# Kernel tuning notes

Measured on AMD Instinct MI355X. Metric: run time of the kernel, lower is better.

## Reference

```python
import jax, jax.numpy as jnp
import numpy as np

T = 100      # sequence length / output times
B = 2048     # batch
DT = 0.02    # euler step == spacing of ts -> one step per interval
CLAMP = 6.0
LOG2PI = float(np.log(2.0 * np.pi))
sp = jax.nn.softplus


def setup_inputs() -> dict:
    key = jax.random.key(0)
    ks = jax.random.split(key, 20)
    rn = lambda k, s, sc=1.0: jax.random.normal(k, s, dtype=jnp.float32) * sc
    inp = {}
    inp['xs'] = rn(ks[0], (T, B, 3, 50))
    inp['ts'] = jnp.arange(T, dtype=jnp.float32) * DT
    inp['eps0'] = rn(ks[1], (B, 6))
    inp['dW'] = rn(ks[2], (T - 1, B, 6)) * np.sqrt(DT)  # Brownian increments ~ N(0, dt)
    # encoder: 150->30->30->15
    inp['eW1'] = rn(ks[3], (150, 30), 150 ** -0.5); inp['eb1'] = jnp.zeros((30,), jnp.float32)
    inp['eW2'] = rn(ks[4], (30, 30), 30 ** -0.5);   inp['eb2'] = jnp.zeros((30,), jnp.float32)
    inp['eW3'] = rn(ks[5], (30, 15), 30 ** -0.5);   inp['eb3'] = jnp.zeros((15,), jnp.float32)
    # decoder: 6->30->30->100
    inp['dcW1'] = rn(ks[6], (6, 30), 6 ** -0.5);    inp['dcb1'] = jnp.zeros((30,), jnp.float32)
    inp['dcW2'] = rn(ks[7], (30, 30), 30 ** -0.5);  inp['dcb2'] = jnp.zeros((30,), jnp.float32)
    inp['dcW3'] = rn(ks[8], (30, 100), 30 ** -0.5); inp['dcb3'] = jnp.zeros((100,), jnp.float32)
    # f_net: (6+1+3)=10 -> 30 -> 6
    inp['fW1'] = rn(ks[9], (10, 30), 10 ** -0.5);   inp['fb1'] = jnp.zeros((30,), jnp.float32)
    inp['fW2'] = rn(ks[10], (30, 6), 30 ** -0.5);   inp['fb2'] = jnp.zeros((6,), jnp.float32)
    # h_net: (6+1)=7 -> 30 -> 6
    inp['hW1'] = rn(ks[11], (7, 30), 7 ** -0.5);    inp['hb1'] = jnp.zeros((30,), jnp.float32)
    inp['hW2'] = rn(ks[12], (30, 6), 30 ** -0.5);   inp['hb2'] = jnp.zeros((6,), jnp.float32)
    # 6 g_nets stacked: 2 -> 30 -> 1 (sigmoid)
    inp['gW1'] = rn(ks[13], (6, 2, 30), 2 ** -0.5); inp['gb1'] = jnp.zeros((6, 30), jnp.float32)
    inp['gW2'] = rn(ks[14], (6, 30, 1), 30 ** -0.5); inp['gb2'] = jnp.zeros((6, 1), jnp.float32)
    inp['pz0_mean'] = jnp.zeros((1, 6), jnp.float32)
    inp['pz0_logstd'] = jnp.zeros((1, 6), jnp.float32)
    return inp


def _forward(xs, ts, eps0, dW, eW1, eb1, eW2, eb2, eW3, eb3,
             dcW1, dcb1, dcW2, dcb2, dcW3, dcb3,
             fW1, fb1, fW2, fb2, hW1, hb1, hW2, hb2,
             gW1, gb1, gW2, gb2, pz0_mean, pz0_logstd):
    # ---- encoder on time-reversed xs ----
    xse = jnp.flip(xs, 0).reshape(T, B, 150)
    e = sp(xse @ eW1 + eb1)
    e = sp(e @ eW2 + eb2)
    e = e @ eW3 + eb3                         # [T,B,15]
    qz0_mean = e[-1, :, :6]
    qz0_logstd = e[-1, :, 6:12]
    ctx = jnp.flip(e[..., 12:15], 0)           # [T,B,3]

    z0 = qz0_mean + jnp.exp(jnp.clip(qz0_logstd, -CLAMP, CLAMP)) * eps0

    # ---- Euler-Maruyama with logqp (one step per ts interval) ----
    def step(z, sc):
        k, dWk = sc
        t = ts[k]
        dtk = ts[k + 1] - ts[k]
        c = ctx[jnp.minimum(k + 1, T - 1)]     # searchsorted(ts, t, right=True) clamped
        tb = jnp.broadcast_to(t, (B, 1)).astype(z.dtype)
        f = sp(jnp.concatenate([tb, z, c], 1) @ fW1 + fb1) @ fW2 + fb2
        h = sp(jnp.concatenate([tb, z], 1) @ hW1 + hb1) @ hW2 + hb2
        gin = jnp.stack([jnp.broadcast_to(t, (B, 6)).astype(z.dtype), z], -1)  # [B,6,2]
        gh = sp(jnp.einsum('bdi,dih->bdh', gin, gW1) + gb1)
        g = jax.nn.sigmoid(jnp.einsum('bdh,dho->bdo', gh, gW2) + gb2)[..., 0]  # [B,6]
        u = (f - h) / g
        logr = 0.5 * jnp.sum(u * u, axis=1) * dtk   # [B]
        zn = z + f * dtk + g * dWk
        return zn, (zn, logr)

    _, (zs_tail, log_ratio) = jax.lax.scan(step, z0, (jnp.arange(T - 1), dW))
    zs = jnp.concatenate([z0[None], zs_tail], 0)   # [T,B,6]

    # ---- decoder + likelihood ----
    d = sp(zs @ dcW1 + dcb1)
    d = sp(d @ dcW2 + dcb2)
    d = d @ dcW3 + dcb3                        # [T,B,100]
    xm, xl = d[..., :50], d[..., 50:]
    xsig = jnp.exp(jnp.clip(xl, -CLAMP, CLAMP))
    tgt = xs[:, :, -1, :]
    lp = -0.5 * ((tgt - xm) / xsig) ** 2 - jnp.log(xsig) - 0.5 * LOG2PI
    log_pxs = jnp.mean(jnp.sum(lp, axis=(0, 2)))

    # ---- KL(q(z0)||p(z0)) + path term ----
    sq = jnp.exp(jnp.clip(qz0_logstd, -CLAMP, CLAMP))
    spz = jnp.exp(jnp.clip(pz0_logstd, -CLAMP, CLAMP))
    kl = jnp.log(spz / sq) + (sq ** 2 + (qz0_mean - pz0_mean) ** 2) / (2.0 * spz ** 2) - 0.5
    logqp0 = jnp.mean(jnp.sum(kl, axis=1))
    logqp_path = jnp.mean(jnp.sum(log_ratio, axis=0))
    return log_pxs, logqp0 + logqp_path


def reference(xs, ts, eps0, dW, eW1, eb1, eW2, eb2, eW3, eb3,
              dcW1, dcb1, dcW2, dcb2, dcW3, dcb3,
              fW1, fb1, fW2, fb2, hW1, hb1, hW2, hb2,
              gW1, gb1, gW2, gb2, pz0_mean, pz0_logstd):
    return _forward(xs, ts, eps0, dW, eW1, eb1, eW2, eb2, eW3, eb3,
                    dcW1, dcb1, dcW2, dcb2, dcW3, dcb3,
                    fW1, fb1, fW2, fb2, hW1, hb1, hW2, hb2,
                    gW1, gb1, gW2, gb2, pz0_mean, pz0_logstd)
```

## Files before the change

kernel.cpp:

```cpp
#include <hip/hip_runtime.h>
#include <hip/hip_bf16.h>
#include <math.h>

#define Tn 100
#define Bn 2048

typedef int v2i __attribute__((ext_vector_type(2)));

__device__ __forceinline__ float sp_f(float x) {
    float e = __expf(-fabsf(x));
    return fmaxf(x, 0.f) + __logf(1.f + e);
}
__device__ __forceinline__ float clamp6(float x) {
    return fminf(fmaxf(x, -6.f), 6.f);
}
__device__ __forceinline__ float dpp_xor1(float x) {
    return __int_as_float(__builtin_amdgcn_mov_dpp(__float_as_int(x), 0xB1, 0xF, 0xF, 1));
}
__device__ __forceinline__ float dpp_xor2(float x) {
    return __int_as_float(__builtin_amdgcn_mov_dpp(__float_as_int(x), 0x4E, 0xF, 0xF, 1));
}
__device__ __forceinline__ float dpp_hmirror(float x) {
    return __int_as_float(__builtin_amdgcn_mov_dpp(__float_as_int(x), 0x141, 0xF, 0xF, 1));
}
__device__ __forceinline__ float dpp_ror8(float x) {
    return __int_as_float(__builtin_amdgcn_mov_dpp(__float_as_int(x), 0x128, 0xF, 0xF, 1));
}
template <int OFF>
__device__ __forceinline__ float swz(float x) {
    return __int_as_float(__builtin_amdgcn_ds_swizzle(__float_as_int(x), OFF));
}
__device__ __forceinline__ float xor16_sum(float x) {
#if __has_builtin(__builtin_amdgcn_permlane16_swap)
    v2i r = __builtin_amdgcn_permlane16_swap(__float_as_int(x), __float_as_int(x), false, false);
    return __int_as_float(r[0]) + __int_as_float(r[1]);
#else
    return x + swz<0x401F>(x);
#endif
}
__device__ __forceinline__ float other_half(float x) {
#if __has_builtin(__builtin_amdgcn_permlane32_swap)
    v2i r = __builtin_amdgcn_permlane32_swap(__float_as_int(x), __float_as_int(x), false, false);
    return (__int_as_float(r[0]) + __int_as_float(r[1])) - x;
#else
    return __shfl_xor(x, 32);
#endif
}

__device__ __forceinline__ void row2(float* ha, float* hb, const float* wrow,
                                     float va, float vb) {
#pragma unroll
    for (int q = 0; q < 7; ++q) {
        float4 wv = *(const float4*)(wrow + 4 * q);
        ha[4 * q + 0] = fmaf(va, wv.x, ha[4 * q + 0]);
        hb[4 * q + 0] = fmaf(vb, wv.x, hb[4 * q + 0]);
        ha[4 * q + 1] = fmaf(va, wv.y, ha[4 * q + 1]);
        hb[4 * q + 1] = fmaf(vb, wv.y, hb[4 * q + 1]);
        ha[4 * q + 2] = fmaf(va, wv.z, ha[4 * q + 2]);
        hb[4 * q + 2] = fmaf(vb, wv.z, hb[4 * q + 2]);
        ha[4 * q + 3] = fmaf(va, wv.w, ha[4 * q + 3]);
        hb[4 * q + 3] = fmaf(vb, wv.w, hb[4 * q + 3]);
    }
    float2 wt = *(const float2*)(wrow + 28);
    ha[28] = fmaf(va, wt.x, ha[28]);
    hb[28] = fmaf(vb, wt.x, hb[28]);
    ha[29] = fmaf(va, wt.y, ha[29]);
    hb[29] = fmaf(vb, wt.y, hb[29]);
}
__device__ __forceinline__ void dot30_2(const float* ha, const float* hb,
                                        const float* wrow, float& ra, float& rb) {
    float a0 = 0.f, a1 = 0.f, b0 = 0.f, b1 = 0.f;
#pragma unroll
    for (int q = 0; q < 7; ++q) {
        float4 wv = *(const float4*)(wrow + 4 * q);
        a0 = fmaf(ha[4 * q + 0], wv.x, a0);
        b0 = fmaf(hb[4 * q + 0], wv.x, b0);
        a1 = fmaf(ha[4 * q + 1], wv.y, a1);
        b1 = fmaf(hb[4 * q + 1], wv.y, b1);
        a0 = fmaf(ha[4 * q + 2], wv.z, a0);
        b0 = fmaf(hb[4 * q + 2], wv.z, b0);
        a1 = fmaf(ha[4 * q + 3], wv.w, a1);
        b1 = fmaf(hb[4 * q + 3], wv.w, b1);
    }
    float2 wt = *(const float2*)(wrow + 28);
    a0 = fmaf(ha[28], wt.x, a0);
    b0 = fmaf(hb[28], wt.x, b0);
    a1 = fmaf(ha[29], wt.y, a1);
    b1 = fmaf(hb[29], wt.y, b1);
    ra = a0 + a1; rb = b0 + b1;
}

#define ENC_LOAD2(b0, b1, base)                                               \
    _Pragma("unroll")                                                         \
    for (int i = 0; i < 5; ++i) {                                             \
        b0[i] = *(const float2*)(x0 + (base) + 2 * i);                        \
        b1[i] = *(const float2*)(x1 + (base) + 2 * i);                        \
    }
#define ENC_COMP2(b0, b1, base)                                               \
    _Pragma("unroll")                                                         \
    for (int i = 0; i < 5; ++i) {                                             \
        row2(h1a, h1b, &w[(base + 2 * i) * 32], b0[i].x, b1[i].x);            \
        row2(h1a, h1b, &w[(base + 2 * i + 1) * 32], b0[i].y, b1[i].y);        \
    }

__global__ __launch_bounds__(256) void enc_kernel(
    const float* __restrict__ xs,
    const float* __restrict__ eW1, const float* __restrict__ eb1,
    const float* __restrict__ eW2, const float* __restrict__ eb2,
    const float* __restrict__ eW3, const float* __restrict__ eb3,
    float* __restrict__ ctx, float* __restrict__ qm, float* __restrict__ qs)
{
    __shared__ float w[6292];
    for (int i = threadIdx.x; i < 4500; i += 256) w[(i / 30) * 32 + (i % 30)] = eW1[i];
    if (threadIdx.x < 30) w[4800 + threadIdx.x] = eb1[threadIdx.x];
    for (int i = threadIdx.x; i < 900; i += 256) w[4832 + (i / 30) * 32 + (i % 30)] = eW2[i];
    if (threadIdx.x < 30) w[5792 + threadIdx.x] = eb2[threadIdx.x];
    for (int i = threadIdx.x; i < 450; i += 256) w[5824 + i] = eW3[i];
    if (threadIdx.x < 15) w[6274 + threadIdx.x] = eb3[threadIdx.x];
    __syncthreads();

    int t = threadIdx.x;
    size_t base = (size_t)blockIdx.x * 512;
    size_t s0 = base + t, s1 = base + t + 256;
    const float* x0 = xs + s0 * 150;
    const float* x1 = xs + s1 * 150;

    float h1a[30], h1b[30];
#pragma unroll
    for (int j = 0; j < 30; ++j) { h1a[j] = w[4800 + j]; h1b[j] = h1a[j]; }

    float2 A0[5], A1[5], B0[5], B1[5];
    ENC_LOAD2(A0, A1, 0)
    ENC_LOAD2(B0, B1, 10)
    int fb = 0;
#pragma unroll 1
    for (int it = 0; it < 6; ++it) {
        ENC_COMP2(A0, A1, fb)
        ENC_LOAD2(A0, A1, fb + 20)
        ENC_COMP2(B0, B1, fb + 10)
        ENC_LOAD2(B0, B1, fb + 30)
        fb += 20;
    }
    ENC_COMP2(A0, A1, 120)
    ENC_LOAD2(A0, A1, 140)
    ENC_COMP2(B0, B1, 130)
    ENC_COMP2(A0, A1, 140)

#pragma unroll
    for (int j = 0; j < 30; ++j) { h1a[j] = sp_f(h1a[j]); h1b[j] = sp_f(h1b[j]); }

    float h2a[30], h2b[30];
#pragma unroll
    for (int j = 0; j < 30; ++j) { h2a[j] = w[5792 + j]; h2b[j] = h2a[j]; }
#pragma unroll
    for (int j1 = 0; j1 < 30; ++j1)
        row2(h2a, h2b, &w[4832 + j1 * 32], h1a[j1], h1b[j1]);
#pragma unroll
    for (int j = 0; j < 30; ++j) { h2a[j] = sp_f(h2a[j]); h2b[j] = sp_f(h2b[j]); }

    float oa12 = w[6274 + 12], oa13 = w[6274 + 13], oa14 = w[6274 + 14];
    float ob12 = oa12, ob13 = oa13, ob14 = oa14;
#pragma unroll
    for (int j2 = 0; j2 < 30; ++j2) {
        float w12 = w[5824 + j2 * 15 + 12];
        float w13 = w[5824 + j2 * 15 + 13];
        float w14 = w[5824 + j2 * 15 + 14];
        oa12 = fmaf(h2a[j2], w12, oa12); ob12 = fmaf(h2b[j2], w12, ob12);
        oa13 = fmaf(h2a[j2], w13, oa13); ob13 = fmaf(h2b[j2], w13, ob13);
        oa14 = fmaf(h2a[j2], w14, oa14); ob14 = fmaf(h2b[j2], w14, ob14);
    }
    float* cp0 = ctx + s0 * 3;
    cp0[0] = oa12; cp0[1] = oa13; cp0[2] = oa14;
    float* cp1 = ctx + s1 * 3;
    cp1[0] = ob12; cp1[1] = ob13; cp1[2] = ob14;

    if (blockIdx.x < 4) {
        float oa[12], ob[12];
#pragma unroll
        for (int j3 = 0; j3 < 12; ++j3) { oa[j3] = w[6274 + j3]; ob[j3] = oa[j3]; }
#pragma unroll
        for (int j2 = 0; j2 < 30; ++j2) {
            float hva = h2a[j2], hvb = h2b[j2];
#pragma unroll
            for (int j3 = 0; j3 < 12; ++j3) {
                float wv = w[5824 + j2 * 15 + j3];
                oa[j3] = fmaf(hva, wv, oa[j3]);
                ob[j3] = fmaf(hvb, wv, ob[j3]);
            }
        }
#pragma unroll
        for (int d = 0; d < 6; ++d) {
            qm[s0 * 6 + d] = oa[d]; qs[s0 * 6 + d] = oa[6 + d];
            qm[s1 * 6 + d] = ob[d]; qs[s1 * 6 + d] = ob[6 + d];
        }
    }
}

__global__ __launch_bounds__(128, 4) void scan_kernel(
    const float* __restrict__ ts, const float* __restrict__ dWall,
    const float* __restrict__ fW1, const float* __restrict__ fb1,
    const float* __restrict__ fW2, const float* __restrict__ fb2,
    const float* __restrict__ hW1, const float* __restrict__ hb1,
    const float* __restrict__ hW2, const float* __restrict__ hb2,
    const float* __restrict__ gW1, const float* __restrict__ gb1,
    const float* __restrict__ gW2, const float* __restrict__ gb2,
    const float* __restrict__ ctx,
    const float* __restrict__ qm, const float* __restrict__ qs,
    const float* __restrict__ eps0, const float* __restrict__ pm,
    const float* __restrict__ ps,
    float* __restrict__ zsb, float* __restrict__ acc)
{
    int tid = threadIdx.x;
    int lane = tid & 63;
    int b = blockIdx.x;
    bool isA = tid < 64;

    __shared__ float sRec[99 * 12];
    __shared__ float exF[2][16];
    __shared__ float exG[2][16];

    for (int i = tid; i < 99 * 3; i += 128) {
        int k = i / 3, e = i % 3;
        float2 v = *(const float2*)(dWall + ((size_t)k * Bn + b) * 6 + e * 2);
        *(float2*)&sRec[k * 12 + e * 2] = v;
    }
    for (int i = tid; i < 99 * 3; i += 128) {
        int k = i / 3, e = i % 3;
        sRec[k * 12 + 6 + e] = ctx[((size_t)(k + 1) * Bn + b) * 3 + e];
    }
    for (int i = tid; i < 99; i += 128) {
        float t0 = ts[i], t1 = ts[i + 1];
        sRec[i * 12 + 9]  = t0;
        sRec[i * 12 + 10] = t1 - t0;
        sRec[i * 12 + 11] = 0.f;
    }

    float z[6];
#pragma unroll
    for (int d = 0; d < 6; ++d) {
        float m = qm[b * 6 + d];
        float sq = __expf(clamp6(qs[b * 6 + d]));
        z[d] = fmaf(sq, eps0[b * 6 + d], m);
    }
    if (tid == 0) {
        float* zp = zsb + (size_t)b * 6;
        *(float2*)(zp)     = make_float2(z[0], z[1]);
        *(float2*)(zp + 2) = make_float2(z[2], z[3]);
        *(float2*)(zp + 4) = make_float2(z[4], z[5]);
    }
    if (tid == 64) {
        float klsum = 0.f;
#pragma unroll
        for (int d = 0; d < 6; ++d) {
            float m = qm[b * 6 + d];
            float sq = __expf(clamp6(qs[b * 6 + d]));
            float spz = __expf(clamp6(ps[d]));
            float dm = m - pm[d];
            klsum += __logf(spz / sq) + (sq * sq + dm * dm) / (2.f * spz * spz) - 0.5f;
        }
        atomicAdd(&acc[1], klsum);
    }

    float wl1[10], b1w, wl2[6], fb2v[6], hb2v[6];
    float gwa[4], gwb[4], gw2v[4], gbb[4], gb2v;
    int dL = 0;
    if (isA) {
        bool lower = lane < 32;
        int j = lane & 31;
        int jc = (j < 30) ? j : 29;
        bool jvalid = (j < 30);
#pragma unroll
        for (int i = 0; i < 10; ++i)
            wl1[i] = lower ? fW1[i * 30 + jc] : (i < 7 ? hW1[i * 30 + jc] : 0.f);
        b1w = lower ? fb1[jc] : hb1[jc];
#pragma unroll
        for (int d = 0; d < 6; ++d)
            wl2[d] = jvalid ? (lower ? fW2[jc * 6 + d] : hW2[jc * 6 + d]) : 0.f;
#pragma unroll
        for (int d = 0; d < 6; ++d) { fb2v[d] = fb2[d]; hb2v[d] = hb2[d]; }
    } else {
        int dL8 = lane >> 3;
        dL = (dL8 < 6) ? dL8 : 0;
        int s = lane & 7;
#pragma unroll
        for (int u = 0; u < 4; ++u) {
            int jj = s + 8 * u;
            bool ok = (dL8 < 6) && (jj < 30);
            gwa[u]  = ok ? gW1[dL * 60 + jj] : 0.f;
            gwb[u]  = ok ? gW1[dL * 60 + 30 + jj] : 0.f;
            gw2v[u] = ok ? gW2[dL * 30 + jj] : 0.f;
            gbb[u]  = ok ? gb1[dL * 30 + jj] : 0.f;
        }
        gb2v = gb2[dL];
    }

    __syncthreads();

    float pacc = 0.f;

    for (int k = 0; k < Tn - 1; ++k) {
        int kb = k & 1;
        float4 r0 = *(float4*)&sRec[k * 12];
        float4 r1 = *(float4*)&sRec[k * 12 + 4];
        float4 r2 = *(float4*)&sRec[k * 12 + 8];
        float t = r2.y, dt = r2.z;

        if (isA) {
            float a = fmaf(t, wl1[0], b1w);
#pragma unroll
            for (int i = 0; i < 6; ++i) a = fmaf(z[i], wl1[1 + i], a);
            a = fmaf(r1.z, wl1[7], a);
            a = fmaf(r1.w, wl1[8], a);
            a = fmaf(r2.x, wl1[9], a);
            float hid = sp_f(a);

            float pp[6];
#pragma unroll
            for (int d = 0; d < 6; ++d) pp[d] = hid * wl2[d];
#pragma unroll
            for (int d = 0; d < 6; ++d) pp[d] += dpp_xor1(pp[d]);
#pragma unroll
            for (int d = 0; d < 6; ++d) pp[d] += dpp_xor2(pp[d]);
#pragma unroll
            for (int d = 0; d < 6; ++d) pp[d] += dpp_hmirror(pp[d]);
#pragma unroll
            for (int d = 0; d < 6; ++d) pp[d] += dpp_ror8(pp[d]);
#pragma unroll
            for (int d = 0; d < 6; ++d) pp[d] = xor16_sum(pp[d]);
            float fvv[6], dfh[6];
            bool lower = lane < 32;
#pragma unroll
            for (int d = 0; d < 6; ++d) {
                float oth = other_half(pp[d]);
                float fsum = lower ? pp[d] : oth;
                float hsum = lower ? oth : pp[d];
                fvv[d] = fsum + fb2v[d];
                dfh[d] = fvv[d] - (hsum + hb2v[d]);
            }
            if (lane == 0) {
                *(float4*)&exF[kb][0] = make_float4(fvv[0], fvv[1], fvv[2], fvv[3]);
                *(float4*)&exF[kb][4] = make_float4(fvv[4], fvv[5], dfh[0], dfh[1]);
                *(float4*)&exF[kb][8] = make_float4(dfh[2], dfh[3], dfh[4], dfh[5]);
            }
        } else {
            float zq = z[0];
            zq = (dL == 1) ? z[1] : zq;
            zq = (dL == 2) ? z[2] : zq;
            zq = (dL == 3) ? z[3] : zq;
            zq = (dL == 4) ? z[4] : zq;
            zq = (dL == 5) ? z[5] : zq;
            float ga = 0.f;
#pragma unroll
            for (int u = 0; u < 4; ++u) {
                float pre = fmaf(t, gwa[u], gbb[u]);
                pre = fmaf(zq, gwb[u], pre);
                ga = fmaf(sp_f(pre), gw2v[u], ga);
            }
            ga += dpp_xor1(ga);
            ga += dpp_xor2(ga);
            ga += dpp_hmirror(ga);
            float gacc = ga + gb2v;
            float e = __expf(-gacc);
            float rg = 1.f + e;
            float gval = __builtin_amdgcn_rcpf(rg);
            if ((lane & 7) == 0 && (lane >> 3) < 6)
                *(float2*)&exG[kb][2 * dL] = make_float2(gval, rg);
        }

        __syncthreads();

        float4 f03 = *(float4*)&exF[kb][0];
        float4 f47 = *(float4*)&exF[kb][4];
        float4 d25 = *(float4*)&exF[kb][8];
        float4 e01 = *(float4*)&exG[kb][0];
        float4 e23 = *(float4*)&exG[kb][4];
        float4 e45 = *(float4*)&exG[kb][8];
        float fvv[6] = { f03.x, f03.y, f03.z, f03.w, f47.x, f47.y };
        float dfh[6] = { f47.z, f47.w, d25.x, d25.y, d25.z, d25.w };
        float gl[6]  = { e01.x, e01.z, e23.x, e23.z, e45.x, e45.z };
        float rgv[6] = { e01.y, e01.w, e23.y, e23.w, e45.y, e45.w };

        if (!isA) {
            float s2 = 0.f;
#pragma unroll
            for (int d = 0; d < 6; ++d) {
                float u = dfh[d] * rgv[d];
                s2 = fmaf(u, u, s2);
            }
            pacc = fmaf(0.5f * dt, s2, pacc);
        }

        float dwv[6] = { r0.x, r0.y, r0.z, r0.w, r1.x, r1.y };
#pragma unroll
        for (int d = 0; d < 6; ++d)
            z[d] = fmaf(gl[d], dwv[d], fmaf(fvv[d], dt, z[d]));

        if (tid == 0) {
            float* zp = zsb + ((size_t)(k + 1) * Bn + b) * 6;
            *(float2*)(zp)     = make_float2(z[0], z[1]);
            *(float2*)(zp + 2) = make_float2(z[2], z[3]);
            *(float2*)(zp + 4) = make_float2(z[4], z[5]);
        }
    }
    if (tid == 64) atomicAdd(&acc[2], pacc);
}

#define DEC_TLOAD(b0, b1, base)                                               \
    _Pragma("unroll")                                                         \
    for (int i = 0; i < 5; ++i) {                                             \
        b0[i] = *(const float2*)(tg0 + (base) + 2 * i);                       \
        b1[i] = *(const float2*)(tg1 + (base) + 2 * i);                       \
    }
#define DEC_LCOMP(b0, b1, base)                                               \
    _Pragma("unroll")                                                         \
    for (int i = 0; i < 10; ++i) {                                            \
        int ff = (base) + i;                                                  \
        float dma, dmb, dla, dlb;                                             \
        dot30_2(h2a, h2b, &w[1216 + ff * 32], dma, dmb);                      \
        dot30_2(h2a, h2b, &w[1216 + (50 + ff) * 32], dla, dlb);               \
        float xma = w[4416 + ff] + dma, xmb = w[4416 + ff] + dmb;             \
        float cla = clamp6(w[4416 + 50 + ff] + dla);                          \
        float clb = clamp6(w[4416 + 50 + ff] + dlb);                          \
        float tva = (i & 1) ? b0[i >> 1].y : b0[i >> 1].x;                    \
        float tvb = (i & 1) ? b1[i >> 1].y : b1[i >> 1].x;                    \
        float ua = (tva - xma) * __expf(-cla);                                \
        float ub = (tvb - xmb) * __expf(-clb);                                \
        lpa += -0.5f * ua * ua - cla - 0.91893853320467274f;                  \
        lpb += -0.5f * ub * ub - clb - 0.91893853320467274f;                  \
    }

__global__ __launch_bounds__(256) void dec_kernel(
    const float* __restrict__ zsb, const float* __restrict__ xs,
    const float* __restrict__ dcW1, const float* __restrict__ dcb1,
    const float* __restrict__ dcW2, const float* __restrict__ dcb2,
    const float* __restrict__ dcW3, const float* __restrict__ dcb3,
    float* __restrict__ acc)
{
    __shared__ float w[4516];
    for (int i = threadIdx.x; i < 180; i += 256) w[(i / 30) * 32 + (i % 30)] = dcW1[i];
    if (threadIdx.x < 30) w[192 + threadIdx.x] = dcb1[threadIdx.x];
    for (int i = threadIdx.x; i < 900; i += 256) w[224 + (i / 30) * 32 + (i % 30)] = dcW2[i];
    if (threadIdx.x < 30) w[1184 + threadIdx.x] = dcb2[threadIdx.x];
    for (int i = threadIdx.x; i < 3000; i += 256) {
        int j2 = i / 100, j3 = i % 100;
        w[1216 + j3 * 32 + j2] = dcW3[i];
    }
    for (int i = threadIdx.x; i < 100; i += 256) w[4416 + i] = dcb3[i];
    __syncthreads();

    int t = threadIdx.x;
    size_t base = (size_t)blockIdx.x * 512;
    size_t s0 = base + t, s1 = base + t + 256;

    float za[6], zb[6];
    {
        const float* zp0 = zsb + s0 * 6;
        const float* zp1 = zsb + s1 * 6;
#pragma unroll
        for (int i = 0; i < 3; ++i) {
            float2 v0 = *(const float2*)(zp0 + 2 * i);
            float2 v1 = *(const float2*)(zp1 + 2 * i);
            za[2 * i] = v0.x; za[2 * i + 1] = v0.y;
            zb[2 * i] = v1.x; zb[2 * i + 1] = v1.y;
        }
    }

    float h1a[30], h1b[30];
#pragma unroll
    for (int j = 0; j < 30; ++j) { h1a[j] = w[192 + j]; h1b[j] = h1a[j]; }
#pragma unroll
    for (int i = 0; i < 6; ++i) row2(h1a, h1b, &w[i * 32], za[i], zb[i]);
#pragma unroll
    for (int j = 0; j < 30; ++j) { h1a[j] = sp_f(h1a[j]); h1b[j] = sp_f(h1b[j]); }

    float h2a[30], h2b[30];
#pragma unroll
    for (int j = 0; j < 30; ++j) { h2a[j] = w[1184 + j]; h2b[j] = h2a[j]; }
#pragma unroll
    for (int j1 = 0; j1 < 30; ++j1)
        row2(h2a, h2b, &w[224 + j1 * 32], h1a[j1], h1b[j1]);
#pragma unroll
    for (int j = 0; j < 30; ++j) { h2a[j] = sp_f(h2a[j]); h2b[j] = sp_f(h2b[j]); }

    const float* tg0 = xs + s0 * 150 + 100;
    const float* tg1 = xs + s1 * 150 + 100;
    float lpa = 0.f, lpb = 0.f;
    float2 TA0[5], TA1[5], TB0[5], TB1[5];
    DEC_TLOAD(TA0, TA1, 0)
    DEC_TLOAD(TB0, TB1, 10)
    DEC_LCOMP(TA0, TA1, 0)
    DEC_TLOAD(TA0, TA1, 20)
    DEC_LCOMP(TB0, TB1, 10)
    DEC_TLOAD(TB0, TB1, 30)
    DEC_LCOMP(TA0, TA1, 20)
    DEC_TLOAD(TA0, TA1, 40)
    DEC_LCOMP(TB0, TB1, 30)
    DEC_LCOMP(TA0, TA1, 40)

    float lpacc = lpa + lpb;
#pragma unroll
    for (int mm = 1; mm <= 32; mm <<= 1) lpacc += __shfl_xor(lpacc, mm);
    __shared__ float red[4];
    if ((threadIdx.x & 63) == 0) red[threadIdx.x >> 6] = lpacc;
    __syncthreads();
    if (threadIdx.x == 0) atomicAdd(&acc[0], red[0] + red[1] + red[2] + red[3]);
}

__global__ void final_kernel(const float* __restrict__ acc, float* __restrict__ out)
{
    out[0] = acc[0] * (1.f / (float)Bn);
    out[1] = (acc[1] + acc[2]) * (1.f / (float)Bn);
}

extern "C" void kernel_launch(void* const* d_in, const int* in_sizes, int n_in,
                              void* d_out, int out_size, void* d_ws, size_t ws_size,
                              hipStream_t stream)
{
    const float* xs   = (const float*)d_in[0];
    const float* ts   = (const float*)d_in[1];
    const float* eps0 = (const float*)d_in[2];
    const float* dW   = (const float*)d_in[3];
    const float* eW1  = (const float*)d_in[4];
    const float* eb1  = (const float*)d_in[5];
    const float* eW2  = (const float*)d_in[6];
    const float* eb2  = (const float*)d_in[7];
    const float* eW3  = (const float*)d_in[8];
    const float* eb3  = (const float*)d_in[9];
    const float* dcW1 = (const float*)d_in[10];
    const float* dcb1 = (const float*)d_in[11];
    const float* dcW2 = (const float*)d_in[12];
    const float* dcb2 = (const float*)d_in[13];
    const float* dcW3 = (const float*)d_in[14];
    const float* dcb3 = (const float*)d_in[15];
    const float* fW1  = (const float*)d_in[16];
    const float* fb1  = (const float*)d_in[17];
    const float* fW2  = (const float*)d_in[18];
    const float* fb2  = (const float*)d_in[19];
    const float* hW1  = (const float*)d_in[20];
    const float* hb1  = (const float*)d_in[21];
    const float* hW2  = (const float*)d_in[22];
    const float* hb2  = (const float*)d_in[23];
    const float* gW1  = (const float*)d_in[24];
    const float* gb1  = (const float*)d_in[25];
    const float* gW2  = (const float*)d_in[26];
    const float* gb2  = (const float*)d_in[27];
    const float* pm   = (const float*)d_in[28];
    const float* ps   = (const float*)d_in[29];

    float* ws  = (float*)d_ws;
    float* acc = ws;
    float* ctx = ws + 16;
    float* qm  = ctx + 614400;
    float* qs  = qm + 12288;
    float* zs  = qs + 12288;
    float* out = (float*)d_out;

    hipMemsetAsync(acc, 0, 16 * sizeof(float), stream);
    enc_kernel<<<400, 256, 0, stream>>>(xs, eW1, eb1, eW2, eb2, eW3, eb3, ctx, qm, qs);
    scan_kernel<<<2048, 128, 0, stream>>>(ts, dW, fW1, fb1, fW2, fb2, hW1, hb1,
                                          hW2, hb2, gW1, gb1, gW2, gb2, ctx,
                                          qm, qs, eps0, pm, ps, zs, acc);
    dec_kernel<<<400, 256, 0, stream>>>(zs, xs, dcW1, dcb1, dcW2, dcb2, dcW3, dcb3, acc);
    final_kernel<<<1, 1, 0, stream>>>(acc, out);
}
```

Measured before the change: 258.0 us.

## Split f_net and h_net across separate wavefronts in scan kernel

```diff
diff --git a/kernel.cpp b/kernel.cpp
--- a/kernel.cpp
+++ b/kernel.cpp
@@ -38,12 +38,12 @@
     return x + swz<0x401F>(x);
 #endif
 }
-__device__ __forceinline__ float other_half(float x) {
+__device__ __forceinline__ float xor32_sum(float x) {
 #if __has_builtin(__builtin_amdgcn_permlane32_swap)
     v2i r = __builtin_amdgcn_permlane32_swap(__float_as_int(x), __float_as_int(x), false, false);
-    return (__int_as_float(r[0]) + __int_as_float(r[1])) - x;
+    return __int_as_float(r[0]) + __int_as_float(r[1]);
 #else
-    return __shfl_xor(x, 32);
+    return x + __shfl_xor(x, 32);
 #endif
 }
 
@@ -196,7 +196,7 @@
     }
 }
 
-__global__ __launch_bounds__(128, 4) void scan_kernel(
+__global__ __launch_bounds__(192, 6) void scan_kernel(
     const float* __restrict__ ts, const float* __restrict__ dWall,
     const float* __restrict__ fW1, const float* __restrict__ fb1,
     const float* __restrict__ fW2, const float* __restrict__ fb2,
@@ -212,23 +212,24 @@
 {
     int tid = threadIdx.x;
     int lane = tid & 63;
+    int wid = tid >> 6;
     int b = blockIdx.x;
-    bool isA = tid < 64;
 
     __shared__ float sRec[99 * 12];
-    __shared__ float exF[2][16];
+    __shared__ float exF[2][8];
+    __shared__ float exH[2][8];
     __shared__ float exG[2][16];
 
-    for (int i = tid; i < 99 * 3; i += 128) {
+    for (int i = tid; i < 99 * 3; i += 192) {
         int k = i / 3, e = i % 3;
         float2 v = *(const float2*)(dWall + ((size_t)k * Bn + b) * 6 + e * 2);
         *(float2*)&sRec[k * 12 + e * 2] = v;
     }
-    for (int i = tid; i < 99 * 3; i += 128) {
+    for (int i = tid; i < 99 * 3; i += 192) {
         int k = i / 3, e = i % 3;
         sRec[k * 12 + 6 + e] = ctx[((size_t)(k + 1) * Bn + b) * 3 + e];
     }
-    for (int i = tid; i < 99; i += 128) {
+    for (int i = tid; i < 99; i += 192) {
         float t0 = ts[i], t1 = ts[i + 1];
         sRec[i * 12 + 9]  = t0;
         sRec[i * 12 + 10] = t1 - t0;
@@ -261,23 +262,33 @@
         atomicAdd(&acc[1], klsum);
     }
 
-    float wl1[10], b1w, wl2[6], fb2v[6], hb2v[6];
+    float wl1[10], b1w, wl2[6], bias2[6];
     float gwa[4], gwb[4], gw2v[4], gbb[4], gb2v;
     int dL = 0;
-    if (isA) {
-        bool lower = lane < 32;
-        int j = lane & 31;
-        int jc = (j < 30) ? j : 29;
-        bool jvalid = (j < 30);
-#pragma unroll
-        for (int i = 0; i < 10; ++i)
-            wl1[i] = lower ? fW1[i * 30 + jc] : (i < 7 ? hW1[i * 30 + jc] : 0.f);
-        b1w = lower ? fb1[jc] : hb1[jc];
-#pragma unroll
-        for (int d = 0; d < 6; ++d)
-            wl2[d] = jvalid ? (lower ? fW2[jc * 6 + d] : hW2[jc * 6 + d]) : 0.f;
-#pragma unroll
-        for (int d = 0; d < 6; ++d) { fb2v[d] = fb2[d]; hb2v[d] = hb2[d]; }
+    if (wid == 0) {
+        int jc = (lane < 30) ? lane : 29;
+        bool jvalid = (lane < 30);
+#pragma unroll
+        for (int i = 0; i < 10; ++i) wl1[i] = fW1[i * 30 + jc];
+        b1w = fb1[jc];
+#pragma unroll
+        for (int d = 0; d < 6; ++d) {
+            wl2[d] = jvalid ? fW2[jc * 6 + d] : 0.f;
+            bias2[d] = fb2[d];
+        }
+    } else if (wid == 1) {
+        int jc = (lane < 30) ? lane : 29;
+        bool jvalid = (lane < 30);
+#pragma unroll
+        for (int i = 0; i < 7; ++i) wl1[i] = hW1[i * 30 + jc];
+#pragma unroll
+        for (int i = 7; i < 10; ++i) wl1[i] = 0.f;
+        b1w = hb1[jc];
+#pragma unroll
+        for (int d = 0; d < 6; ++d) {
+            wl2[d] = jvalid ? hW2[jc * 6 + d] : 0.f;
+            bias2[d] = hb2[d];
+        }
     } else {
         int dL8 = lane >> 3;
         dL = (dL8 < 6) ? dL8 : 0;
@@ -305,7 +316,7 @@
         float4 r2 = *(float4*)&sRec[k * 12 + 8];
         float t = r2.y, dt = r2.z;
 
-        if (isA) {
+        if (wid < 2) {
             float a = fmaf(t, wl1[0], b1w);
 #pragma unroll
             for (int i = 0; i < 6; ++i) a = fmaf(z[i], wl1[1 + i], a);
@@ -327,20 +338,12 @@
             for (int d = 0; d < 6; ++d) pp[d] += dpp_ror8(pp[d]);
 #pragma unroll
             for (int d = 0; d < 6; ++d) pp[d] = xor16_sum(pp[d]);
-            float fvv[6], dfh[6];
-            bool lower = lane < 32;
-#pragma unroll
-            for (int d = 0; d < 6; ++d) {
-                float oth = other_half(pp[d]);
-                float fsum = lower ? pp[d] : oth;
-                float hsum = lower ? oth : pp[d];
-                fvv[d] = fsum + fb2v[d];
-                dfh[d] = fvv[d] - (hsum + hb2v[d]);
-            }
+#pragma unroll
+            for (int d = 0; d < 6; ++d) pp[d] = xor32_sum(pp[d]) + bias2[d];
             if (lane == 0) {
-                *(float4*)&exF[kb][0] = make_float4(fvv[0], fvv[1], fvv[2], fvv[3]);
-                *(float4*)&exF[kb][4] = make_float4(fvv[4], fvv[5], dfh[0], dfh[1]);
-                *(float4*)&exF[kb][8] = make_float4(dfh[2], dfh[3], dfh[4], dfh[5]);
+                float* ex = (wid == 0) ? &exF[kb][0] : &exH[kb][0];
+                *(float4*)(ex)     = make_float4(pp[0], pp[1], pp[2], pp[3]);
+                *(float2*)(ex + 4) = make_float2(pp[4], pp[5]);
             }
         } else {
             float zq = z[0];
@@ -369,22 +372,23 @@
 
         __syncthreads();
 
-        float4 f03 = *(float4*)&exF[kb][0];
-        float4 f47 = *(float4*)&exF[kb][4];
-        float4 d25 = *(float4*)&exF[kb][8];
+        float4 fA = *(float4*)&exF[kb][0];
+        float2 fB = *(float2*)&exF[kb][4];
+        float4 hA = *(float4*)&exH[kb][0];
+        float2 hB = *(float2*)&exH[kb][4];
         float4 e01 = *(float4*)&exG[kb][0];
         float4 e23 = *(float4*)&exG[kb][4];
         float4 e45 = *(float4*)&exG[kb][8];
-        float fvv[6] = { f03.x, f03.y, f03.z, f03.w, f47.x, f47.y };
-        float dfh[6] = { f47.z, f47.w, d25.x, d25.y, d25.z, d25.w };
+        float fvv[6] = { fA.x, fA.y, fA.z, fA.w, fB.x, fB.y };
+        float hvv[6] = { hA.x, hA.y, hA.z, hA.w, hB.x, hB.y };
         float gl[6]  = { e01.x, e01.z, e23.x, e23.z, e45.x, e45.z };
-        float rgv[6] = { e01.y, e01.w, e23.y, e23.w, e45.y, e45.w };
-
-        if (!isA) {
+
+        if (wid == 2) {
+            float rgv[6] = { e01.y, e01.w, e23.y, e23.w, e45.y, e45.w };
             float s2 = 0.f;
 #pragma unroll
             for (int d = 0; d < 6; ++d) {
-                float u = dfh[d] * rgv[d];
+                float u = (fvv[d] - hvv[d]) * rgv[d];
                 s2 = fmaf(u, u, s2);
             }
             pacc = fmaf(0.5f * dt, s2, pacc);
@@ -402,7 +406,7 @@
             *(float2*)(zp + 4) = make_float2(z[4], z[5]);
         }
     }
-    if (tid == 64) atomicAdd(&acc[2], pacc);
+    if (tid == 128) atomicAdd(&acc[2], pacc);
 }
 
 #define DEC_TLOAD(b0, b1, base)                                               \
@@ -557,7 +561,7 @@
 
     hipMemsetAsync(acc, 0, 16 * sizeof(float), stream);
     enc_kernel<<<400, 256, 0, stream>>>(xs, eW1, eb1, eW2, eb2, eW3, eb3, ctx, qm, qs);
-    scan_kernel<<<2048, 128, 0, stream>>>(ts, dW, fW1, fb1, fW2, fb2, hW1, hb1,
+    scan_kernel<<<2048, 192, 0, stream>>>(ts, dW, fW1, fb1, fW2, fb2, hW1, hb1,
                                           hW2, hb2, gW1, gb1, gW2, gb2, ctx,
                                           qm, qs, eps0, pm, ps, zs, acc);
     dec_kernel<<<400, 256, 0, stream>>>(zs, xs, dcW1, dcb1, dcW2, dcb2, dcW3, dcb3, acc);
```

Measured after the change: 303.8 us. +17.8%, slower.

## Specialize SDE loop per wave: g-wave tracks single latent dim, trims LDS exchange

Applied to the files above, without the earlier changes.

```diff
diff --git a/kernel.cpp b/kernel.cpp
--- a/kernel.cpp
+++ b/kernel.cpp
@@ -216,8 +216,8 @@
     bool isA = tid < 64;
 
     __shared__ float sRec[99 * 12];
-    __shared__ float exF[2][16];
-    __shared__ float exG[2][16];
+    __shared__ float exF[2][12];
+    __shared__ float exG[2][8];
 
     for (int i = tid; i < 99 * 3; i += 128) {
         int k = i / 3, e = i % 3;
@@ -230,40 +230,17 @@
     }
     for (int i = tid; i < 99; i += 128) {
         float t0 = ts[i], t1 = ts[i + 1];
-        sRec[i * 12 + 9]  = t0;
-        sRec[i * 12 + 10] = t1 - t0;
-        sRec[i * 12 + 11] = 0.f;
+        sRec[i * 12 + 9]  = 0.f;
+        sRec[i * 12 + 10] = t0;
+        sRec[i * 12 + 11] = t1 - t0;
     }
 
     float z[6];
-#pragma unroll
-    for (int d = 0; d < 6; ++d) {
-        float m = qm[b * 6 + d];
-        float sq = __expf(clamp6(qs[b * 6 + d]));
-        z[d] = fmaf(sq, eps0[b * 6 + d], m);
-    }
-    if (tid == 0) {
-        float* zp = zsb + (size_t)b * 6;
-        *(float2*)(zp)     = make_float2(z[0], z[1]);
-        *(float2*)(zp + 2) = make_float2(z[2], z[3]);
-        *(float2*)(zp + 4) = make_float2(z[4], z[5]);
-    }
-    if (tid == 64) {
-        float klsum = 0.f;
-#pragma unroll
-        for (int d = 0; d < 6; ++d) {
-            float m = qm[b * 6 + d];
-            float sq = __expf(clamp6(qs[b * 6 + d]));
-            float spz = __expf(clamp6(ps[d]));
-            float dm = m - pm[d];
-            klsum += __logf(spz / sq) + (sq * sq + dm * dm) / (2.f * spz * spz) - 0.5f;
-        }
-        atomicAdd(&acc[1], klsum);
-    }
-
+    float zq = 0.f;
     float wl1[10], b1w, wl2[6], fb2v[6], hb2v[6];
-    float gwa[4], gwb[4], gw2v[4], gbb[4], gb2v;
+    float gwa[4], gwb[4], gw2v[4], gbb[4], gb2v = 0.f, wselq = 0.f;
     int dL = 0;
+
     if (isA) {
         bool lower = lane < 32;
         int j = lane & 31;
@@ -278,9 +255,22 @@
             wl2[d] = jvalid ? (lower ? fW2[jc * 6 + d] : hW2[jc * 6 + d]) : 0.f;
 #pragma unroll
         for (int d = 0; d < 6; ++d) { fb2v[d] = fb2[d]; hb2v[d] = hb2[d]; }
+#pragma unroll
+        for (int d = 0; d < 6; ++d) {
+            float m = qm[b * 6 + d];
+            float sq = __expf(clamp6(qs[b * 6 + d]));
+            z[d] = fmaf(sq, eps0[b * 6 + d], m);
+        }
+        if (tid == 0) {
+            float* zp = zsb + (size_t)b * 6;
+            *(float2*)(zp)     = make_float2(z[0], z[1]);
+            *(float2*)(zp + 2) = make_float2(z[2], z[3]);
+            *(float2*)(zp + 4) = make_float2(z[4], z[5]);
+        }
     } else {
         int dL8 = lane >> 3;
         dL = (dL8 < 6) ? dL8 : 0;
+        wselq = (dL8 < 6) ? 0.0625f : 0.f;
         int s = lane & 7;
 #pragma unroll
         for (int u = 0; u < 4; ++u) {
@@ -292,6 +282,23 @@
             gbb[u]  = ok ? gb1[dL * 30 + jj] : 0.f;
         }
         gb2v = gb2[dL];
+        {
+            float m = qm[b * 6 + dL];
+            float sq = __expf(clamp6(qs[b * 6 + dL]));
+            zq = fmaf(sq, eps0[b * 6 + dL], m);
+        }
+        if (tid == 64) {
+            float klsum = 0.f;
+#pragma unroll
+            for (int d = 0; d < 6; ++d) {
+                float m = qm[b * 6 + d];
+                float sq = __expf(clamp6(qs[b * 6 + d]));
+                float spz = __expf(clamp6(ps[d]));
+                float dm = m - pm[d];
+                klsum += __logf(spz / sq) + (sq * sq + dm * dm) / (2.f * spz * spz) - 0.5f;
+            }
+            atomicAdd(&acc[1], klsum);
+        }
     }
 
     __syncthreads();
@@ -300,12 +307,13 @@
 
     for (int k = 0; k < Tn - 1; ++k) {
         int kb = k & 1;
-        float4 r0 = *(float4*)&sRec[k * 12];
-        float4 r1 = *(float4*)&sRec[k * 12 + 4];
-        float4 r2 = *(float4*)&sRec[k * 12 + 8];
-        float t = r2.y, dt = r2.z;
 
         if (isA) {
+            float4 r0 = *(float4*)&sRec[k * 12];
+            float4 r1 = *(float4*)&sRec[k * 12 + 4];
+            float4 r2 = *(float4*)&sRec[k * 12 + 8];
+            float t = r2.z, dt = r2.w;
+
             float a = fmaf(t, wl1[0], b1w);
 #pragma unroll
             for (int i = 0; i < 6; ++i) a = fmaf(z[i], wl1[1 + i], a);
@@ -342,13 +350,28 @@
                 *(float4*)&exF[kb][4] = make_float4(fvv[4], fvv[5], dfh[0], dfh[1]);
                 *(float4*)&exF[kb][8] = make_float4(dfh[2], dfh[3], dfh[4], dfh[5]);
             }
+
+            __syncthreads();
+
+            float4 g03 = *(float4*)&exG[kb][0];
+            float2 g45 = *(float2*)&exG[kb][4];
+            float gl[6] = { g03.x, g03.y, g03.z, g03.w, g45.x, g45.y };
+            float dwv[6] = { r0.x, r0.y, r0.z, r0.w, r1.x, r1.y };
+#pragma unroll
+            for (int d = 0; d < 6; ++d)
+                z[d] = fmaf(gl[d], dwv[d], fmaf(fvv[d], dt, z[d]));
+
+            if (tid == 0) {
+                float* zp = zsb + ((size_t)(k + 1) * Bn + b) * 6;
+                *(float2*)(zp)     = make_float2(z[0], z[1]);
+                *(float2*)(zp + 2) = make_float2(z[2], z[3]);
+                *(float2*)(zp + 4) = make_float2(z[4], z[5]);
+            }
         } else {
-            float zq = z[0];
-            zq = (dL == 1) ? z[1] : zq;
-            zq = (dL == 2) ? z[2] : zq;
-            zq = (dL == 3) ? z[3] : zq;
-            zq = (dL == 4) ? z[4] : zq;
-            zq = (dL == 5) ? z[5] : zq;
+            float2 tdt = *(float2*)&sRec[k * 12 + 10];
+            float t = tdt.x, dt = tdt.y;
+            float dwq = sRec[k * 12 + dL];
+
             float ga = 0.f;
 #pragma unroll
             for (int u = 0; u < 4; ++u) {
@@ -364,45 +387,22 @@
             float rg = 1.f + e;
             float gval = __builtin_amdgcn_rcpf(rg);
             if ((lane & 7) == 0 && (lane >> 3) < 6)
-                *(float2*)&exG[kb][2 * dL] = make_float2(gval, rg);
-        }
-
-        __syncthreads();
-
-        float4 f03 = *(float4*)&exF[kb][0];
-        float4 f47 = *(float4*)&exF[kb][4];
-        float4 d25 = *(float4*)&exF[kb][8];
-        float4 e01 = *(float4*)&exG[kb][0];
-        float4 e23 = *(float4*)&exG[kb][4];
-        float4 e45 = *(float4*)&exG[kb][8];
-        float fvv[6] = { f03.x, f03.y, f03.z, f03.w, f47.x, f47.y };
-        float dfh[6] = { f47.z, f47.w, d25.x, d25.y, d25.z, d25.w };
-        float gl[6]  = { e01.x, e01.z, e23.x, e23.z, e45.x, e45.z };
-        float rgv[6] = { e01.y, e01.w, e23.y, e23.w, e45.y, e45.w };
-
-        if (!isA) {
-            float s2 = 0.f;
-#pragma unroll
-            for (int d = 0; d < 6; ++d) {
-                float u = dfh[d] * rgv[d];
-                s2 = fmaf(u, u, s2);
-            }
-            pacc = fmaf(0.5f * dt, s2, pacc);
-        }
-
-        float dwv[6] = { r0.x, r0.y, r0.z, r0.w, r1.x, r1.y };
-#pragma unroll
-        for (int d = 0; d < 6; ++d)
-            z[d] = fmaf(gl[d], dwv[d], fmaf(fvv[d], dt, z[d]));
-
-        if (tid == 0) {
-            float* zp = zsb + ((size_t)(k + 1) * Bn + b) * 6;
-            *(float2*)(zp)     = make_float2(z[0], z[1]);
-            *(float2*)(zp + 2) = make_float2(z[2], z[3]);
-            *(float2*)(zp + 4) = make_float2(z[4], z[5]);
-        }
-    }
-    if (tid == 64) atomicAdd(&acc[2], pacc);
+                exG[kb][dL] = gval;
+
+            __syncthreads();
+
+            float fq  = exF[kb][dL];
+            float dfq = exF[kb][6 + dL];
+            float u = dfq * rg;
+            pacc = fmaf(wselq * dt, u * u, pacc);
+            zq = fmaf(gval, dwq, fmaf(fq, dt, zq));
+        }
+    }
+    if (!isA) {
+#pragma unroll
+        for (int mm = 1; mm <= 32; mm <<= 1) pacc += __shfl_xor(pacc, mm);
+        if (tid == 64) atomicAdd(&acc[2], pacc);
+    }
 }
 
 #define DEC_TLOAD(b0, b1, base)                                               \
```

Result: no change. 253.5 us (-1.8%).
